# Performance work log

Hardware: AMD Instinct MI355X
Metric: run time of the kernel (lower is better)

## Reference

```python
import jax, jax.numpy as jnp
import numpy as np
import math

B, T, C, H = 4, 2048, 1024, 16

def setup_inputs() -> dict:
    key = jax.random.key(0)
    ks = jax.random.split(key, 9)
    s = 0.02
    return {
        "x":  jax.random.normal(ks[0], (B, T, C), dtype=jnp.float32),
        "Wq": jax.random.normal(ks[1], (C, C), dtype=jnp.float32) * s,
        "bq": jax.random.normal(ks[2], (C,), dtype=jnp.float32) * s,
        "Wk": jax.random.normal(ks[3], (C, C), dtype=jnp.float32) * s,
        "bk": jax.random.normal(ks[4], (C,), dtype=jnp.float32) * s,
        "Wv": jax.random.normal(ks[5], (C, C), dtype=jnp.float32) * s,
        "bv": jax.random.normal(ks[6], (C,), dtype=jnp.float32) * s,
        "Wp": jax.random.normal(ks[7], (C, C), dtype=jnp.float32) * s,
        "bp": jax.random.normal(ks[8], (C,), dtype=jnp.float32) * s,
    }

def reference(x, Wq, bq, Wk, bk, Wv, bv, Wp, bp):
    b, t, c = x.shape
    h = H
    d = c // h
    # torch Linear: y = x @ W.T + b
    q = (x @ Wq.T + bq).reshape(b, t, h, d).transpose(0, 2, 1, 3)  # [B,H,T,d]
    k = (x @ Wk.T + bk).reshape(b, t, h, d).transpose(0, 2, 1, 3)
    v = (x @ Wv.T + bv).reshape(b, t, h, d).transpose(0, 2, 1, 3)
    att = jnp.einsum('bhqd,bhkd->bhqk', q, k) * (1.0 / math.sqrt(d))  # [B,H,T,T]
    causal = jnp.tril(jnp.ones((t, t), dtype=bool))
    att = jnp.where(causal[None, None, :, :], att, -jnp.inf)
    att = jax.nn.softmax(att, axis=-1)
    # attn_drop / resid_drop are identity in eval mode
    y = jnp.einsum('bhqk,bhkd->bhqd', att, v)        # [B,H,T,d]
    y = y.transpose(0, 2, 1, 3).reshape(b, t, c)      # [B,T,C]
    y = y @ Wp.T + bp
    return y
```

## Files before the change

### kernel.cpp

```cpp
#include <hip/hip_runtime.h>
#include <hip/hip_bf16.h>

typedef __attribute__((ext_vector_type(8))) short bf16x8;
typedef __attribute__((ext_vector_type(4))) float f32x4;

struct bf16x8_s { __hip_bfloat16 h[8]; };
struct bf16x4_s { __hip_bfloat16 h[4]; };

__global__ void cvt_kernel(const float* __restrict__ in,
                           __hip_bfloat16* __restrict__ out, int n8) {
  int i = blockIdx.x * blockDim.x + threadIdx.x;
  if (i >= n8) return;
  const float4* p = reinterpret_cast<const float4*>(in) + (size_t)i * 2;
  float4 a = p[0], b = p[1];
  bf16x8_s o;
  o.h[0] = __float2bfloat16(a.x); o.h[1] = __float2bfloat16(a.y);
  o.h[2] = __float2bfloat16(a.z); o.h[3] = __float2bfloat16(a.w);
  o.h[4] = __float2bfloat16(b.x); o.h[5] = __float2bfloat16(b.y);
  o.h[6] = __float2bfloat16(b.z); o.h[7] = __float2bfloat16(b.w);
  *reinterpret_cast<bf16x8_s*>(out + (size_t)i * 8) = o;
}

__global__ void cvt4_kernel(const float* __restrict__ w0,
                            const float* __restrict__ w1,
                            const float* __restrict__ w2,
                            const float* __restrict__ w3,
                            __hip_bfloat16* __restrict__ out) {
  const int bid = blockIdx.x;
  const int seg = bid >> 9;
  const int i = (bid & 511) * 256 + threadIdx.x;
  const float* src = seg == 0 ? w0 : seg == 1 ? w1 : seg == 2 ? w2 : w3;
  const float4* p = reinterpret_cast<const float4*>(src) + (size_t)i * 2;
  float4 a = p[0], b = p[1];
  bf16x8_s o;
  o.h[0] = __float2bfloat16(a.x); o.h[1] = __float2bfloat16(a.y);
  o.h[2] = __float2bfloat16(a.z); o.h[3] = __float2bfloat16(a.w);
  o.h[4] = __float2bfloat16(b.x); o.h[5] = __float2bfloat16(b.y);
  o.h[6] = __float2bfloat16(b.z); o.h[7] = __float2bfloat16(b.w);
  *reinterpret_cast<bf16x8_s*>(out + (size_t)seg * 1048576 + (size_t)i * 8) = o;
}

__device__ __forceinline__ void stage_tile(const __hip_bfloat16* src,
                                           char* lds, int tid) {
#pragma unroll
  for (int s = 0; s < 4; ++s) {
    const int c = s * 256 + tid;
    const int row = c >> 3;
    const int cb = (((c & 7) << 4) ^ ((row & 7) << 4));
    __builtin_amdgcn_global_load_lds(
        (const __attribute__((address_space(1))) void*)((const char*)(src + (size_t)row * 1024) + cb),
        (__attribute__((address_space(3))) void*)(lds + s * 4096 + (tid & 192) * 16),
        16, 0, 0);
  }
}

template <int MODE>
__global__ __launch_bounds__(256) void gemm128(
    const __hip_bfloat16* __restrict__ A, const __hip_bfloat16* __restrict__ W,
    const float* __restrict__ b0, const float* __restrict__ b1,
    const float* __restrict__ b2, void* __restrict__ O0,
    void* __restrict__ O1, void* __restrict__ O2) {
  constexpr float SC = 0.18033688011112042f;
  __shared__ char smem[32768];
  const int tid = threadIdx.x;
  const int lane = tid & 63;
  const int lrow = lane & 15;
  const int lhi = lane >> 4;
  const int wid = tid >> 6;
  const int wm = wid >> 1, wn = wid & 1;
  const int xr = (lrow & 7) << 4;

  const int n = blockIdx.x;
  int tm, tn;
  if constexpr (MODE == 0) {
    const int xcd = n & 7;
    const int u = n >> 3;
    tn = xcd * 3 + u % 3;
    tm = u / 3;
  } else {
    const int wg = (n & 7) * 64 + (n >> 3);
    tm = wg & 63;
    tn = wg >> 6;
  }
  const int row0 = tm * 128;

  const __hip_bfloat16* Ap = A + (size_t)row0 * 1024;
  const __hip_bfloat16* Wp = W + (size_t)(tn * 128) * 1024;

  f32x4 acc[4][4] = {};

  for (int k0 = 0; k0 < 1024; k0 += 64) {
    stage_tile(Ap + k0, smem, tid);
    stage_tile(Wp + k0, smem + 16384, tid);
    __syncthreads();
    bf16x8 af[4][2], bfr[4][2];
#pragma unroll
    for (int m = 0; m < 4; ++m) {
      const int ar = wm * 64 + m * 16 + lrow;
#pragma unroll
      for (int kk = 0; kk < 2; ++kk)
        af[m][kk] = *reinterpret_cast<const bf16x8*>(
            smem + ar * 128 + ((kk * 64 + lhi * 16) ^ xr));
    }
#pragma unroll
    for (int nn = 0; nn < 4; ++nn) {
      const int br = wn * 64 + nn * 16 + lrow;
#pragma unroll
      for (int kk = 0; kk < 2; ++kk)
        bfr[nn][kk] = *reinterpret_cast<const bf16x8*>(
            smem + 16384 + br * 128 + ((kk * 64 + lhi * 16) ^ xr));
    }
    __builtin_amdgcn_s_setprio(1);
#pragma unroll
    for (int kk = 0; kk < 2; ++kk)
#pragma unroll
      for (int m = 0; m < 4; ++m)
#pragma unroll
        for (int nn = 0; nn < 4; ++nn)
          acc[m][nn] = __builtin_amdgcn_mfma_f32_16x16x32_bf16(
              af[m][kk], bfr[nn][kk], acc[m][nn], 0, 0, 0);
    __builtin_amdgcn_s_setprio(0);
    __syncthreads();
  }

  char* epi = smem + wid * 8192;
  const int grow0 = row0 + wm * 64;

  if constexpr (MODE == 0) {
    const int sel = tn >> 3;
    const int cloc = (tn & 7) * 128 + wn * 64;
    const float* bias = sel == 0 ? b0 : sel == 1 ? b1 : b2;
    float bv4[4];
#pragma unroll
    for (int nn = 0; nn < 4; ++nn) bv4[nn] = bias[cloc + nn * 16 + lrow];

    if (sel != 2) {
      __hip_bfloat16* dst = sel == 0 ? (__hip_bfloat16*)O0 : (__hip_bfloat16*)O1;
#pragma unroll
      for (int mg = 0; mg < 4; ++mg) {
#pragma unroll
        for (int nn = 0; nn < 4; ++nn)
#pragma unroll
          for (int i = 0; i < 4; ++i) {
            float v = acc[mg][nn][i] + bv4[nn];
            if (sel == 0) v *= SC;
            ((__hip_bfloat16*)epi)[(lhi * 4 + i) * 72 + nn * 16 + lrow] =
                __float2bfloat16(v);
          }
#pragma unroll
        for (int ps = 0; ps < 2; ++ps) {
          const int r = ps * 8 + (lane >> 3);
          bf16x8 val = *reinterpret_cast<const bf16x8*>(epi + r * 144 + (lane & 7) * 16);
          const int grow = grow0 + mg * 16 + r;
          *reinterpret_cast<bf16x8*>(&dst[(size_t)grow * 1024 + cloc + (lane & 7) * 8]) = val;
        }
      }
    } else {
      __hip_bfloat16* dst = (__hip_bfloat16*)O2;
      const int h = cloc >> 6;
      const int bb = grow0 >> 11;
      const int t0 = grow0 & 2047;
      __hip_bfloat16* vb = dst + ((size_t)(bb * 16 + h) * 64) * 2048;
#pragma unroll
      for (int ng = 0; ng < 4; ++ng) {
#pragma unroll
        for (int m = 0; m < 4; ++m)
#pragma unroll
          for (int i = 0; i < 4; ++i) {
            const float v = acc[m][ng][i] + bv4[ng];
            ((__hip_bfloat16*)epi)[lrow * 72 + m * 16 + lhi * 4 + i] =
                __float2bfloat16(v);
          }
#pragma unroll
        for (int ps = 0; ps < 2; ++ps) {
          const int dr = ps * 8 + (lane >> 3);
          bf16x8 val = *reinterpret_cast<const bf16x8*>(epi + dr * 144 + (lane & 7) * 16);
          const int d = ng * 16 + dr;
          *reinterpret_cast<bf16x8*>(&vb[(size_t)d * 2048 + t0 + (lane & 7) * 8]) = val;
        }
      }
    }
  } else {
    float* dst = (float*)O0;
    const int cloc = tn * 128 + wn * 64;
    float bv4[4];
#pragma unroll
    for (int nn = 0; nn < 4; ++nn) bv4[nn] = b0[cloc + nn * 16 + lrow];
#pragma unroll
    for (int mg = 0; mg < 4; ++mg) {
#pragma unroll
      for (int nn = 0; nn < 4; ++nn)
#pragma unroll
        for (int i = 0; i < 4; ++i)
          ((float*)epi)[(lhi * 4 + i) * 68 + nn * 16 + lrow] =
              acc[mg][nn][i] + bv4[nn];
#pragma unroll
      for (int ps = 0; ps < 4; ++ps) {
        const int r = ps * 4 + (lane >> 4);
        float4 val = *reinterpret_cast<const float4*>(epi + r * 272 + (lane & 15) * 16);
        const int grow = grow0 + mg * 16 + r;
        *reinterpret_cast<float4*>(&dst[(size_t)grow * 1024 + cloc + (lane & 15) * 4]) = val;
      }
    }
  }
}

__device__ __forceinline__ void stage_kv(char* __restrict__ smem, int buf,
                                         const __hip_bfloat16* __restrict__ Kb,
                                         const __hip_bfloat16* __restrict__ Vb,
                                         int kv0, int tid) {
  const int w = tid >> 6, l = tid & 63;
  char* base = smem + buf * 16384;
#pragma unroll
  for (int s = 0; s < 2; ++s) {
    const int c = s * 256 + w * 64 + l;
    const int row = c >> 3;
    const int scb = ((c & 7) << 4) ^ ((row & 7) << 4);
    __builtin_amdgcn_global_load_lds(
        (const __attribute__((address_space(1))) void*)(Kb + (size_t)(kv0 + row) * 1024 + (scb >> 1)),
        (__attribute__((address_space(3))) void*)(base + s * 4096 + w * 1024), 16, 0, 0);
  }
#pragma unroll
  for (int s = 0; s < 2; ++s) {
    const int c = s * 256 + w * 64 + l;
    const int row = c >> 3;
    const int scb = ((c & 7) << 4) ^ ((row & 7) << 4);
    __builtin_amdgcn_global_load_lds(
        (const __attribute__((address_space(1))) void*)(Vb + (size_t)row * 2048 + kv0 + (scb >> 1)),
        (__attribute__((address_space(3))) void*)(base + 8192 + s * 4096 + w * 1024), 16, 0, 0);
  }
}

template <bool MASKED>
__device__ __forceinline__ void attn_step(
    int kv0, int q0w, int lrow, int lhi, const char* __restrict__ kvb,
    const bf16x8 qf[2][2], f32x4 o[2][4], float lp[2],
    char* __restrict__ Pw) {
  const int xr = (lrow & 7) << 4;
  f32x4 s[2][4] = {};
  __builtin_amdgcn_s_setprio(1);
#pragma unroll
  for (int g = 0; g < 4; ++g) {
    const char* rowp = kvb + (g * 16 + lrow) * 128;
#pragma unroll
    for (int kk = 0; kk < 2; ++kk) {
      bf16x8 kf = *reinterpret_cast<const bf16x8*>(rowp + ((kk * 64 + lhi * 16) ^ xr));
#pragma unroll
      for (int j = 0; j < 2; ++j)
        s[j][g] = __builtin_amdgcn_mfma_f32_16x16x32_bf16(kf, qf[j][kk], s[j][g], 0, 0, 0);
    }
  }
  __builtin_amdgcn_s_setprio(0);
  if (MASKED) {
#pragma unroll
    for (int j = 0; j < 2; ++j)
#pragma unroll
      for (int g = 0; g < 4; ++g)
#pragma unroll
        for (int i = 0; i < 4; ++i) {
          const int k = kv0 + g * 16 + lhi * 4 + i;
          if (k > q0w + j * 16 + lrow) s[j][g][i] = -1e30f;
        }
  }
  bf16x8 pf[2][2];
#pragma unroll
  for (int j = 0; j < 2; ++j) {
    float gs[4];
#pragma unroll
    for (int g = 0; g < 4; ++g) {
      bf16x4_s t4;
      float p0 = exp2f(s[j][g][0]);
      float p1 = exp2f(s[j][g][1]);
      float p2 = exp2f(s[j][g][2]);
      float p3 = exp2f(s[j][g][3]);
      t4.h[0] = __float2bfloat16(p0); t4.h[1] = __float2bfloat16(p1);
      t4.h[2] = __float2bfloat16(p2); t4.h[3] = __float2bfloat16(p3);
      gs[g] = (p0 + p1) + (p2 + p3);
      *reinterpret_cast<bf16x4_s*>(Pw + lrow * 128 + ((g * 32 + lhi * 8) ^ xr)) = t4;
    }
    lp[j] += (gs[0] + gs[1]) + (gs[2] + gs[3]);
#pragma unroll
    for (int nn = 0; nn < 2; ++nn)
      pf[j][nn] = *reinterpret_cast<const bf16x8*>(
          Pw + lrow * 128 + ((nn * 64 + lhi * 16) ^ xr));
  }
  __builtin_amdgcn_s_setprio(1);
#pragma unroll
  for (int nn = 0; nn < 2; ++nn)
#pragma unroll
    for (int f = 0; f < 4; ++f) {
      bf16x8 vf = *reinterpret_cast<const bf16x8*>(
          kvb + 8192 + (f * 16 + lrow) * 128 + ((nn * 64 + lhi * 16) ^ xr));
#pragma unroll
      for (int j = 0; j < 2; ++j)
        o[j][f] = __builtin_amdgcn_mfma_f32_16x16x32_bf16(pf[j][nn], vf, o[j][f], 0, 0, 0);
    }
  __builtin_amdgcn_s_setprio(0);
}

__global__ __launch_bounds__(256, 4) void attn_fwd(
    const __hip_bfloat16* __restrict__ Q, const __hip_bfloat16* __restrict__ Km,
    const __hip_bfloat16* __restrict__ Vt, __hip_bfloat16* __restrict__ Y) {
  constexpr int T = 2048, C = 1024, D = 64;
  const int tid = threadIdx.x;
  const int wid = tid >> 6;
  const int lane = tid & 63;
  const int lrow = lane & 15;
  const int lhi = lane >> 4;
  const int n = blockIdx.x;
  const int xcd = n & 7;
  const int w8 = n >> 3;
  const int j2 = w8 >> 5;
  const int r = w8 & 31;
  const int s5 = r >> 3;
  const int bh = xcd * 8 + (r & 7);
  int p;
  if (j2 == 0) p = s5;
  else if (j2 == 1) p = 3 - s5;
  else if (j2 == 2) p = s5 ^ 1;
  else p = 3 - (s5 ^ 1);
  const int qt = 15 - (j2 * 4 + p);
  const int b = bh >> 4, h = bh & 15;
  const int q0w = qt * 128 + wid * 32;

  const __hip_bfloat16* Qb = Q + ((size_t)b * T) * C + h * D;
  const __hip_bfloat16* Kb = Km + ((size_t)b * T) * C + h * D;
  const __hip_bfloat16* Vb = Vt + (size_t)bh * D * T;

  __shared__ char smem[40960];
  char* Pw = smem + 32768 + wid * 2048;

  bf16x8 qf[2][2];
#pragma unroll
  for (int j = 0; j < 2; ++j)
#pragma unroll
    for (int kk = 0; kk < 2; ++kk)
      qf[j][kk] = *reinterpret_cast<const bf16x8*>(
          Qb + (size_t)(q0w + j * 16 + lrow) * C + kk * 32 + lhi * 8);

  f32x4 o[2][4] = {};
  float lp[2] = {0.f, 0.f};

  const int nt = 2 * qt + 2;
  const int ns = (q0w >> 6) + 1;

  stage_kv(smem, 0, Kb, Vb, 0, tid);
  for (int t = 0; t < nt; ++t) {
    __syncthreads();
    if (t + 1 < nt) stage_kv(smem, (t + 1) & 1, Kb, Vb, (t + 1) * 64, tid);
    if (t < ns) {
      const char* kvb = smem + (t & 1) * 16384;
      if (t == ns - 1)
        attn_step<true>(t * 64, q0w, lrow, lhi, kvb, qf, o, lp, Pw);
      else
        attn_step<false>(t * 64, q0w, lrow, lhi, kvb, qf, o, lp, Pw);
    }
  }

#pragma unroll
  for (int j = 0; j < 2; ++j) {
    float l = lp[j];
    l += __shfl_xor(l, 16);
    l += __shfl_xor(l, 32);
    float l4[4];
#pragma unroll
    for (int i = 0; i < 4; ++i) l4[i] = __shfl(l, 4 * lhi + i, 16);
#pragma unroll
    for (int f = 0; f < 4; ++f)
#pragma unroll
      for (int i = 0; i < 4; ++i) {
        const int row = q0w + j * 16 + 4 * lhi + i;
        Y[((size_t)b * T + row) * C + h * D + f * 16 + lrow] =
            __float2bfloat16(o[j][f][i] / l4[i]);
      }
  }
}

extern "C" void kernel_launch(void* const* d_in, const int* in_sizes, int n_in,
                              void* d_out, int out_size, void* d_ws,
                              size_t ws_size, hipStream_t stream) {
  const float* x = (const float*)d_in[0];
  const float* Wq = (const float*)d_in[1];
  const float* bq = (const float*)d_in[2];
  const float* Wk = (const float*)d_in[3];
  const float* bk = (const float*)d_in[4];
  const float* Wv = (const float*)d_in[5];
  const float* bv = (const float*)d_in[6];
  const float* Wp = (const float*)d_in[7];
  const float* bp = (const float*)d_in[8];
  float* out = (float*)d_out;

  __hip_bfloat16* ws = (__hip_bfloat16*)d_ws;
  __hip_bfloat16* xb = ws;
  __hip_bfloat16* wqb = xb + 8388608;
  __hip_bfloat16* wpb = wqb + 3 * 1048576;
  __hip_bfloat16* Qs = wqb + 4 * 1048576;
  __hip_bfloat16* Ks = Qs + 8388608;
  __hip_bfloat16* Vts = Ks + 8388608;
  __hip_bfloat16* Ys = Vts + 8388608;

  cvt_kernel<<<4096, 256, 0, stream>>>(x, xb, 1048576);
  cvt4_kernel<<<2048, 256, 0, stream>>>(Wq, Wk, Wv, Wp, wqb);

  gemm128<0><<<dim3(1536), 256, 0, stream>>>(xb, wqb, bq, bk, bv, Qs, Ks, Vts);

  attn_fwd<<<dim3(1024), 256, 0, stream>>>(Qs, Ks, Vts, Ys);

  gemm128<1><<<dim3(512), 256, 0, stream>>>(Ys, wpb, bp, nullptr, nullptr, out,
                                            nullptr, nullptr);
}
```

Baseline: 152.4 us.

## Replace QKV GEMM with 256x256 double-buffered 8-wave pipelined kernel

Adds a new QKV projection kernel that uses 256x256 output tiles with 512 threads, 128KB of LDS and double-buffered A/B staging. Global-to-LDS loads for the next k-step are interleaved between four MFMA phases, with explicit waitcnt and barriers. This raises arithmetic intensity per tile and hides load latency behind compute. The grid drops from 1536 to 384 blocks, which lowers occupancy and can leave CUs idle in the tail. The output projection is split out into its own non-templated kernel with the same behavior as before.

```diff
diff --git a/kernel.cpp b/kernel.cpp
--- a/kernel.cpp
+++ b/kernel.cpp
@@ -6,6 +6,9 @@
 
 struct bf16x8_s { __hip_bfloat16 h[8]; };
 struct bf16x4_s { __hip_bfloat16 h[4]; };
+
+#define AS1 __attribute__((address_space(1)))
+#define AS3 __attribute__((address_space(3)))
 
 __global__ void cvt_kernel(const float* __restrict__ in,
                            __hip_bfloat16* __restrict__ out, int n8) {
@@ -40,6 +43,217 @@
   *reinterpret_cast<bf16x8_s*>(out + (size_t)seg * 1048576 + (size_t)i * 8) = o;
 }
 
+__device__ __forceinline__ void stage_half256(const __hip_bfloat16* src,
+                                              char* dstbase, int tid) {
+#pragma unroll
+  for (int s = 0; s < 2; ++s) {
+    const int c = s * 512 + tid;
+    const int r = c >> 3;
+    const int cb = ((c & 7) << 4) ^ ((r & 7) << 4);
+    __builtin_amdgcn_global_load_lds(
+        (const AS1 void*)((const char*)(src + (size_t)r * 1024) + cb),
+        (AS3 void*)(dstbase + s * 8192 + (tid & 448) * 16), 16, 0, 0);
+  }
+}
+
+__global__ __launch_bounds__(512, 1) void gemm256_qkv(
+    const __hip_bfloat16* __restrict__ A, const __hip_bfloat16* __restrict__ W,
+    const float* __restrict__ bq, const float* __restrict__ bk,
+    const float* __restrict__ bv, __hip_bfloat16* __restrict__ Qs,
+    __hip_bfloat16* __restrict__ Ks, __hip_bfloat16* __restrict__ Vts) {
+  constexpr float SC = 0.18033688011112042f;
+  __shared__ char smem[131072];
+  const int tid = threadIdx.x;
+  const int lane = tid & 63;
+  const int lrow = lane & 15;
+  const int lhi = lane >> 4;
+  const int wid = tid >> 6;
+  const int wm = wid >> 2;
+  const int wn = wid & 3;
+  const int xr = (lrow & 7) << 4;
+
+  const int n = blockIdx.x;
+  const int xcd = n & 7;
+  const int u = n >> 3;
+  const int tn = u >> 2;
+  const int tm = xcd * 4 + (u & 3);
+  const int row0 = tm * 256;
+
+  const __hip_bfloat16* Ap = A + (size_t)row0 * 1024;
+  const __hip_bfloat16* Wp = W + (size_t)(tn * 256) * 1024;
+
+#define ABUF(d, h) (smem + (d) * 32768 + (h) * 16384)
+#define BBUF(d, h) (smem + 65536 + (d) * 32768 + (h) * 16384)
+
+  f32x4 acc[8][4] = {};
+
+  stage_half256(Ap, ABUF(0, 0), tid);
+  stage_half256(Ap + 128 * 1024, ABUF(0, 1), tid);
+  stage_half256(Wp, BBUF(0, 0), tid);
+  stage_half256(Wp + 128 * 1024, BBUF(0, 1), tid);
+  stage_half256(Wp + 64, BBUF(1, 0), tid);
+  stage_half256(Wp + 128 * 1024 + 64, BBUF(1, 1), tid);
+  asm volatile("s_waitcnt vmcnt(4)" ::: "memory");
+  __builtin_amdgcn_s_barrier();
+
+  for (int t = 0; t < 16; ++t) {
+    const int d = t & 1;
+    const char* Ab = ABUF(d, wm);
+    const char* Bb = BBUF(d, wn >> 1);
+    const int brow0 = (wn & 1) * 64;
+    bf16x8 af[4][2], bf0[2][2], bf1[2][2];
+
+#pragma unroll
+    for (int m = 0; m < 4; ++m)
+#pragma unroll
+      for (int kk = 0; kk < 2; ++kk)
+        af[m][kk] = *reinterpret_cast<const bf16x8*>(
+            Ab + (m * 16 + lrow) * 128 + ((kk * 64 + lhi * 16) ^ xr));
+#pragma unroll
+    for (int nf = 0; nf < 2; ++nf)
+#pragma unroll
+      for (int kk = 0; kk < 2; ++kk)
+        bf0[nf][kk] = *reinterpret_cast<const bf16x8*>(
+            Bb + (brow0 + nf * 16 + lrow) * 128 + ((kk * 64 + lhi * 16) ^ xr));
+    if (t + 1 < 16) stage_half256(Ap + (t + 1) * 64, ABUF(d ^ 1, 0), tid);
+    __builtin_amdgcn_s_barrier();
+    asm volatile("s_waitcnt lgkmcnt(0)" ::: "memory");
+    __builtin_amdgcn_s_setprio(1);
+#pragma unroll
+    for (int kk = 0; kk < 2; ++kk)
+#pragma unroll
+      for (int m = 0; m < 4; ++m)
+#pragma unroll
+        for (int nf = 0; nf < 2; ++nf)
+          acc[m][nf] = __builtin_amdgcn_mfma_f32_16x16x32_bf16(
+              af[m][kk], bf0[nf][kk], acc[m][nf], 0, 0, 0);
+    __builtin_amdgcn_s_setprio(0);
+    __builtin_amdgcn_s_barrier();
+
+#pragma unroll
+    for (int nf = 0; nf < 2; ++nf)
+#pragma unroll
+      for (int kk = 0; kk < 2; ++kk)
+        bf1[nf][kk] = *reinterpret_cast<const bf16x8*>(
+            Bb + (brow0 + 32 + nf * 16 + lrow) * 128 + ((kk * 64 + lhi * 16) ^ xr));
+    if (t + 1 < 16)
+      stage_half256(Ap + 128 * 1024 + (t + 1) * 64, ABUF(d ^ 1, 1), tid);
+    __builtin_amdgcn_s_barrier();
+    asm volatile("s_waitcnt lgkmcnt(0)" ::: "memory");
+    __builtin_amdgcn_s_setprio(1);
+#pragma unroll
+    for (int kk = 0; kk < 2; ++kk)
+#pragma unroll
+      for (int m = 0; m < 4; ++m)
+#pragma unroll
+        for (int nf = 0; nf < 2; ++nf)
+          acc[m][2 + nf] = __builtin_amdgcn_mfma_f32_16x16x32_bf16(
+              af[m][kk], bf1[nf][kk], acc[m][2 + nf], 0, 0, 0);
+    __builtin_amdgcn_s_setprio(0);
+    __builtin_amdgcn_s_barrier();
+
+#pragma unroll
+    for (int m = 0; m < 4; ++m)
+#pragma unroll
+      for (int kk = 0; kk < 2; ++kk)
+        af[m][kk] = *reinterpret_cast<const bf16x8*>(
+            Ab + (64 + m * 16 + lrow) * 128 + ((kk * 64 + lhi * 16) ^ xr));
+    if (t + 2 < 16) stage_half256(Wp + (t + 2) * 64, BBUF(d, 0), tid);
+    __builtin_amdgcn_s_barrier();
+    asm volatile("s_waitcnt lgkmcnt(0)" ::: "memory");
+    __builtin_amdgcn_s_setprio(1);
+#pragma unroll
+    for (int kk = 0; kk < 2; ++kk)
+#pragma unroll
+      for (int m = 0; m < 4; ++m)
+#pragma unroll
+        for (int nf = 0; nf < 2; ++nf)
+          acc[4 + m][2 + nf] = __builtin_amdgcn_mfma_f32_16x16x32_bf16(
+              af[m][kk], bf1[nf][kk], acc[4 + m][2 + nf], 0, 0, 0);
+    __builtin_amdgcn_s_setprio(0);
+    __builtin_amdgcn_s_barrier();
+
+    if (t + 2 < 16)
+      stage_half256(Wp + 128 * 1024 + (t + 2) * 64, BBUF(d, 1), tid);
+    if (t <= 13) { asm volatile("s_waitcnt vmcnt(4)" ::: "memory"); }
+    else         { asm volatile("s_waitcnt vmcnt(0)" ::: "memory"); }
+    __builtin_amdgcn_s_barrier();
+    asm volatile("s_waitcnt lgkmcnt(0)" ::: "memory");
+    __builtin_amdgcn_s_setprio(1);
+#pragma unroll
+    for (int kk = 0; kk < 2; ++kk)
+#pragma unroll
+      for (int m = 0; m < 4; ++m)
+#pragma unroll
+        for (int nf = 0; nf < 2; ++nf)
+          acc[4 + m][nf] = __builtin_amdgcn_mfma_f32_16x16x32_bf16(
+              af[m][kk], bf0[nf][kk], acc[4 + m][nf], 0, 0, 0);
+    __builtin_amdgcn_s_setprio(0);
+    __builtin_amdgcn_s_barrier();
+  }
+  __syncthreads();
+
+  char* epi = smem + wid * 8192;
+  const int sel = tn >> 2;
+  const int cloc = (tn & 3) * 256 + wn * 64;
+  const float* bias = sel == 0 ? bq : sel == 1 ? bk : bv;
+  float bv4[4];
+#pragma unroll
+  for (int nn = 0; nn < 4; ++nn) bv4[nn] = bias[cloc + nn * 16 + lrow];
+
+#pragma unroll
+  for (int mh = 0; mh < 2; ++mh) {
+    const int grow0 = row0 + wm * 128 + mh * 64;
+    if (sel != 2) {
+      __hip_bfloat16* dst = sel == 0 ? Qs : Ks;
+#pragma unroll
+      for (int mg = 0; mg < 4; ++mg) {
+#pragma unroll
+        for (int nn = 0; nn < 4; ++nn)
+#pragma unroll
+          for (int i = 0; i < 4; ++i) {
+            float v = acc[mh * 4 + mg][nn][i] + bv4[nn];
+            if (sel == 0) v *= SC;
+            ((__hip_bfloat16*)epi)[(lhi * 4 + i) * 72 + nn * 16 + lrow] =
+                __float2bfloat16(v);
+          }
+#pragma unroll
+        for (int ps = 0; ps < 2; ++ps) {
+          const int r = ps * 8 + (lane >> 3);
+          bf16x8 val = *reinterpret_cast<const bf16x8*>(epi + r * 144 + (lane & 7) * 16);
+          const int grow = grow0 + mg * 16 + r;
+          *reinterpret_cast<bf16x8*>(&dst[(size_t)grow * 1024 + cloc + (lane & 7) * 8]) = val;
+        }
+      }
+    } else {
+      const int h = cloc >> 6;
+      const int bb = grow0 >> 11;
+      const int t0 = grow0 & 2047;
+      __hip_bfloat16* vb = Vts + ((size_t)(bb * 16 + h) * 64) * 2048;
+#pragma unroll
+      for (int ng = 0; ng < 4; ++ng) {
+#pragma unroll
+        for (int m = 0; m < 4; ++m)
+#pragma unroll
+          for (int i = 0; i < 4; ++i) {
+            const float v = acc[mh * 4 + m][ng][i] + bv4[ng];
+            ((__hip_bfloat16*)epi)[lrow * 72 + m * 16 + lhi * 4 + i] =
+                __float2bfloat16(v);
+          }
+#pragma unroll
+        for (int ps = 0; ps < 2; ++ps) {
+          const int dr = ps * 8 + (lane >> 3);
+          bf16x8 val = *reinterpret_cast<const bf16x8*>(epi + dr * 144 + (lane & 7) * 16);
+          const int dd = ng * 16 + dr;
+          *reinterpret_cast<bf16x8*>(&vb[(size_t)dd * 2048 + t0 + (lane & 7) * 8]) = val;
+        }
+      }
+    }
+  }
+#undef ABUF
+#undef BBUF
+}
+
 __device__ __forceinline__ void stage_tile(const __hip_bfloat16* src,
                                            char* lds, int tid) {
 #pragma unroll
@@ -48,19 +262,14 @@
     const int row = c >> 3;
     const int cb = (((c & 7) << 4) ^ ((row & 7) << 4));
     __builtin_amdgcn_global_load_lds(
-        (const __attribute__((address_space(1))) void*)((const char*)(src + (size_t)row * 1024) + cb),
-        (__attribute__((address_space(3))) void*)(lds + s * 4096 + (tid & 192) * 16),
-        16, 0, 0);
-  }
-}
-
-template <int MODE>
-__global__ __launch_bounds__(256) void gemm128(
+        (const AS1 void*)((const char*)(src + (size_t)row * 1024) + cb),
+        (AS3 void*)(lds + s * 4096 + (tid & 192) * 16), 16, 0, 0);
+  }
+}
+
+__global__ __launch_bounds__(256) void gemm_proj(
     const __hip_bfloat16* __restrict__ A, const __hip_bfloat16* __restrict__ W,
-    const float* __restrict__ b0, const float* __restrict__ b1,
-    const float* __restrict__ b2, void* __restrict__ O0,
-    void* __restrict__ O1, void* __restrict__ O2) {
-  constexpr float SC = 0.18033688011112042f;
+    const float* __restrict__ b0, float* __restrict__ dst) {
   __shared__ char smem[32768];
   const int tid = threadIdx.x;
   const int lane = tid & 63;
@@ -71,17 +280,9 @@
   const int xr = (lrow & 7) << 4;
 
   const int n = blockIdx.x;
-  int tm, tn;
-  if constexpr (MODE == 0) {
-    const int xcd = n & 7;
-    const int u = n >> 3;
-    tn = xcd * 3 + u % 3;
-    tm = u / 3;
-  } else {
-    const int wg = (n & 7) * 64 + (n >> 3);
-    tm = wg & 63;
-    tn = wg >> 6;
-  }
+  const int wg = (n & 7) * 64 + (n >> 3);
+  const int tm = wg & 63;
+  const int tn = wg >> 6;
   const int row0 = tm * 128;
 
   const __hip_bfloat16* Ap = A + (size_t)row0 * 1024;
@@ -125,82 +326,24 @@
 
   char* epi = smem + wid * 8192;
   const int grow0 = row0 + wm * 64;
-
-  if constexpr (MODE == 0) {
-    const int sel = tn >> 3;
-    const int cloc = (tn & 7) * 128 + wn * 64;
-    const float* bias = sel == 0 ? b0 : sel == 1 ? b1 : b2;
-    float bv4[4];
-#pragma unroll
-    for (int nn = 0; nn < 4; ++nn) bv4[nn] = bias[cloc + nn * 16 + lrow];
-
-    if (sel != 2) {
-      __hip_bfloat16* dst = sel == 0 ? (__hip_bfloat16*)O0 : (__hip_bfloat16*)O1;
-#pragma unroll
-      for (int mg = 0; mg < 4; ++mg) {
-#pragma unroll
-        for (int nn = 0; nn < 4; ++nn)
-#pragma unroll
-          for (int i = 0; i < 4; ++i) {
-            float v = acc[mg][nn][i] + bv4[nn];
-            if (sel == 0) v *= SC;
-            ((__hip_bfloat16*)epi)[(lhi * 4 + i) * 72 + nn * 16 + lrow] =
-                __float2bfloat16(v);
-          }
-#pragma unroll
-        for (int ps = 0; ps < 2; ++ps) {
-          const int r = ps * 8 + (lane >> 3);
-          bf16x8 val = *reinterpret_cast<const bf16x8*>(epi + r * 144 + (lane & 7) * 16);
-          const int grow = grow0 + mg * 16 + r;
-          *reinterpret_cast<bf16x8*>(&dst[(size_t)grow * 1024 + cloc + (lane & 7) * 8]) = val;
-        }
-      }
-    } else {
-      __hip_bfloat16* dst = (__hip_bfloat16*)O2;
-      const int h = cloc >> 6;
-      const int bb = grow0 >> 11;
-      const int t0 = grow0 & 2047;
-      __hip_bfloat16* vb = dst + ((size_t)(bb * 16 + h) * 64) * 2048;
-#pragma unroll
-      for (int ng = 0; ng < 4; ++ng) {
-#pragma unroll
-        for (int m = 0; m < 4; ++m)
-#pragma unroll
-          for (int i = 0; i < 4; ++i) {
-            const float v = acc[m][ng][i] + bv4[ng];
-            ((__hip_bfloat16*)epi)[lrow * 72 + m * 16 + lhi * 4 + i] =
-                __float2bfloat16(v);
-          }
-#pragma unroll
-        for (int ps = 0; ps < 2; ++ps) {
-          const int dr = ps * 8 + (lane >> 3);
-          bf16x8 val = *reinterpret_cast<const bf16x8*>(epi + dr * 144 + (lane & 7) * 16);
-          const int d = ng * 16 + dr;
-          *reinterpret_cast<bf16x8*>(&vb[(size_t)d * 2048 + t0 + (lane & 7) * 8]) = val;
-        }
-      }
-    }
-  } else {
-    float* dst = (float*)O0;
-    const int cloc = tn * 128 + wn * 64;
-    float bv4[4];
-#pragma unroll
-    for (int nn = 0; nn < 4; ++nn) bv4[nn] = b0[cloc + nn * 16 + lrow];
-#pragma unroll
-    for (int mg = 0; mg < 4; ++mg) {
-#pragma unroll
-      for (int nn = 0; nn < 4; ++nn)
-#pragma unroll
-        for (int i = 0; i < 4; ++i)
-          ((float*)epi)[(lhi * 4 + i) * 68 + nn * 16 + lrow] =
-              acc[mg][nn][i] + bv4[nn];
-#pragma unroll
-      for (int ps = 0; ps < 4; ++ps) {
-        const int r = ps * 4 + (lane >> 4);
-        float4 val = *reinterpret_cast<const float4*>(epi + r * 272 + (lane & 15) * 16);
-        const int grow = grow0 + mg * 16 + r;
-        *reinterpret_cast<float4*>(&dst[(size_t)grow * 1024 + cloc + (lane & 15) * 4]) = val;
-      }
+  const int cloc = tn * 128 + wn * 64;
+  float bv4[4];
+#pragma unroll
+  for (int nn = 0; nn < 4; ++nn) bv4[nn] = b0[cloc + nn * 16 + lrow];
+#pragma unroll
+  for (int mg = 0; mg < 4; ++mg) {
+#pragma unroll
+    for (int nn = 0; nn < 4; ++nn)
+#pragma unroll
+      for (int i = 0; i < 4; ++i)
+        ((float*)epi)[(lhi * 4 + i) * 68 + nn * 16 + lrow] =
+            acc[mg][nn][i] + bv4[nn];
+#pragma unroll
+    for (int ps = 0; ps < 4; ++ps) {
+      const int r = ps * 4 + (lane >> 4);
+      float4 val = *reinterpret_cast<const float4*>(epi + r * 272 + (lane & 15) * 16);
+      const int grow = grow0 + mg * 16 + r;
+      *reinterpret_cast<float4*>(&dst[(size_t)grow * 1024 + cloc + (lane & 15) * 4]) = val;
     }
   }
 }
@@ -217,8 +360,8 @@
     const int row = c >> 3;
     const int scb = ((c & 7) << 4) ^ ((row & 7) << 4);
     __builtin_amdgcn_global_load_lds(
-        (const __attribute__((address_space(1))) void*)(Kb + (size_t)(kv0 + row) * 1024 + (scb >> 1)),
-        (__attribute__((address_space(3))) void*)(base + s * 4096 + w * 1024), 16, 0, 0);
+        (const AS1 void*)(Kb + (size_t)(kv0 + row) * 1024 + (scb >> 1)),
+        (AS3 void*)(base + s * 4096 + w * 1024), 16, 0, 0);
   }
 #pragma unroll
   for (int s = 0; s < 2; ++s) {
@@ -226,8 +369,8 @@
     const int row = c >> 3;
     const int scb = ((c & 7) << 4) ^ ((row & 7) << 4);
     __builtin_amdgcn_global_load_lds(
-        (const __attribute__((address_space(1))) void*)(Vb + (size_t)row * 2048 + kv0 + (scb >> 1)),
-        (__attribute__((address_space(3))) void*)(base + 8192 + s * 4096 + w * 1024), 16, 0, 0);
+        (const AS1 void*)(Vb + (size_t)row * 2048 + kv0 + (scb >> 1)),
+        (AS3 void*)(base + 8192 + s * 4096 + w * 1024), 16, 0, 0);
   }
 }
 
@@ -402,10 +545,9 @@
   cvt_kernel<<<4096, 256, 0, stream>>>(x, xb, 1048576);
   cvt4_kernel<<<2048, 256, 0, stream>>>(Wq, Wk, Wv, Wp, wqb);
 
-  gemm128<0><<<dim3(1536), 256, 0, stream>>>(xb, wqb, bq, bk, bv, Qs, Ks, Vts);
+  gemm256_qkv<<<dim3(384), 512, 0, stream>>>(xb, wqb, bq, bk, bv, Qs, Ks, Vts);
 
   attn_fwd<<<dim3(1024), 256, 0, stream>>>(Qs, Ks, Vts, Ys);
 
-  gemm128<1><<<dim3(512), 256, 0, stream>>>(Ys, wpb, bp, nullptr, nullptr, out,
-                                            nullptr, nullptr);
-}
+  gemm_proj<<<dim3(512), 256, 0, stream>>>(Ys, wpb, bp, out);
+}
```

Measured after the change: 155.0 us. About the same (+1.7%).
